# Kernel optimization log

Measured on AMD Instinct MI355X. Metric: run time of the kernel, lower is better.

Reference implementation:

```python
import jax, jax.numpy as jnp
import numpy as np

B, D, L, N = 16384, 128, 20, 1_000_000


def setup_inputs() -> dict:
    key = jax.random.key(0)
    k1, k2, k3, k4 = jax.random.split(key, 4)
    xw = jax.random.normal(k1, (B, D), dtype=jnp.float32)
    # weight table: row i == weight of nn.Linear(n_embs, 1) for node i
    W = jax.random.normal(k2, (N, D), dtype=jnp.float32) * 0.02
    h_path = jax.random.randint(k3, (L,), 0, N, dtype=jnp.int32)
    h_code = jax.random.randint(k4, (L,), 0, 2).astype(jnp.float32)
    return {"xw": xw, "W": W, "h_code": h_code, "h_path": h_path}


def reference(xw, W, h_code, h_path):
    # Gather only the L path rows (mirrors per-node tiny Linear lookups)
    Wp = W[h_path]                      # (L, D)
    z = jnp.einsum("bd,ld->bl", xw, Wp)  # (B, L) logits, one per path node
    # h_code*log(sigmoid(z)) + (1-h_code)*log(1-sigmoid(z)), computed stably:
    # log(sigmoid(z)) = log_sigmoid(z); log(1-sigmoid(z)) = log_sigmoid(-z)
    p = h_code * jax.nn.log_sigmoid(z) + (1.0 - h_code) * jax.nn.log_sigmoid(-z)
    # original sums the list of (B,1) tensors over the path
    return jnp.sum(p, axis=1, keepdims=True)  # (B, 1)
```

## Files before the change

### kernel.cpp

```cpp
#include <hip/hip_runtime.h>
#include <math.h>

#define BB 16384
#define DD 128
#define LL 20

__global__ __launch_bounds__(64) void hs_kernel(
    const float* __restrict__ xw,
    const float* __restrict__ W,
    const float* __restrict__ h_code,
    const int*   __restrict__ h_path,
    float* __restrict__ out)
{
    __shared__ float4 Ws[LL * (DD / 4)];
    __shared__ float  codes[LL];

    const int tid = threadIdx.x;

    for (int i = tid; i < LL * (DD / 4); i += 64) {
        const int l = i >> 5;
        const int c = i & 31;
        const long long row = (long long)h_path[l];
        Ws[i] = ((const float4*)W)[row * (DD / 4) + c];
    }
    if (tid < LL) codes[tid] = h_code[tid];
    __syncthreads();

    const int b = blockIdx.x * 64 + tid;
    const float4* x4 = (const float4*)(xw + (size_t)b * DD);

    float z[LL];
#pragma unroll
    for (int l = 0; l < LL; ++l) z[l] = 0.0f;

#pragma unroll 4
    for (int c = 0; c < DD / 4; ++c) {
        const float4 x = x4[c];
#pragma unroll
        for (int l = 0; l < LL; ++l) {
            const float4 w = Ws[l * (DD / 4) + c];
            z[l] += x.x * w.x + x.y * w.y + x.z * w.z + x.w * w.w;
        }
    }

    float s = 0.0f;
#pragma unroll
    for (int l = 0; l < LL; ++l) {
        const float zl = z[l];
        const float t  = -zl;
        const float sp = fmaxf(t, 0.0f) + log1pf(expf(-fabsf(t)));
        s -= sp + (1.0f - codes[l]) * zl;
    }
    out[b] = s;
}

extern "C" void kernel_launch(void* const* d_in, const int* in_sizes, int n_in,
                              void* d_out, int out_size, void* d_ws, size_t ws_size,
                              hipStream_t stream) {
    const float* xw     = (const float*)d_in[0];
    const float* W      = (const float*)d_in[1];
    const float* h_code = (const float*)d_in[2];
    const int*   h_path = (const int*)d_in[3];
    float* out = (float*)d_out;

    hs_kernel<<<BB / 64, 64, 0, stream>>>(xw, W, h_code, h_path, out);
}
```

Baseline: 567.3 us.

## Split each row's dot products across four threads with shuffle reduction

```diff
diff --git a/kernel.cpp b/kernel.cpp
--- a/kernel.cpp
+++ b/kernel.cpp
@@ -4,8 +4,10 @@
 #define BB 16384
 #define DD 128
 #define LL 20
+#define ROWS_PER_BLOCK 64
+#define THREADS 256
 
-__global__ __launch_bounds__(64) void hs_kernel(
+__global__ __launch_bounds__(THREADS) void hs_kernel(
     const float* __restrict__ xw,
     const float* __restrict__ W,
     const float* __restrict__ h_code,
@@ -17,24 +19,26 @@
 
     const int tid = threadIdx.x;
 
-    for (int i = tid; i < LL * (DD / 4); i += 64) {
+    for (int i = tid; i < LL * (DD / 4); i += THREADS) {
         const int l = i >> 5;
         const int c = i & 31;
-        const long long row = (long long)h_path[l];
-        Ws[i] = ((const float4*)W)[row * (DD / 4) + c];
+        Ws[i] = ((const float4*)W)[(long long)h_path[l] * (DD / 4) + c];
     }
     if (tid < LL) codes[tid] = h_code[tid];
     __syncthreads();
 
-    const int b = blockIdx.x * 64 + tid;
-    const float4* x4 = (const float4*)(xw + (size_t)b * DD);
+    const int p   = tid & 3;
+    const int r   = tid >> 2;
+    const int row = blockIdx.x * ROWS_PER_BLOCK + r;
+    const float4* x4 = (const float4*)xw + (size_t)row * (DD / 4);
 
     float z[LL];
 #pragma unroll
     for (int l = 0; l < LL; ++l) z[l] = 0.0f;
 
-#pragma unroll 4
-    for (int c = 0; c < DD / 4; ++c) {
+#pragma unroll
+    for (int j = 0; j < 8; ++j) {
+        const int c = p + 4 * j;
         const float4 x = x4[c];
 #pragma unroll
         for (int l = 0; l < LL; ++l) {
@@ -43,15 +47,23 @@
         }
     }
 
-    float s = 0.0f;
 #pragma unroll
     for (int l = 0; l < LL; ++l) {
-        const float zl = z[l];
-        const float t  = -zl;
-        const float sp = fmaxf(t, 0.0f) + log1pf(expf(-fabsf(t)));
-        s -= sp + (1.0f - codes[l]) * zl;
+        z[l] += __shfl_xor(z[l], 1);
+        z[l] += __shfl_xor(z[l], 2);
     }
-    out[b] = s;
+
+    if (p == 0) {
+        float s = 0.0f;
+#pragma unroll
+        for (int l = 0; l < LL; ++l) {
+            const float zl = z[l];
+            const float t  = -zl;
+            const float sp = fmaxf(t, 0.0f) + log1pf(expf(-fabsf(t)));
+            s -= sp + (1.0f - codes[l]) * zl;
+        }
+        out[row] = s;
+    }
 }
 
 extern "C" void kernel_launch(void* const* d_in, const int* in_sizes, int n_in,
@@ -63,5 +75,5 @@
     const int*   h_path = (const int*)d_in[3];
     float* out = (float*)d_out;
 
-    hs_kernel<<<BB / 64, 64, 0, stream>>>(xw, W, h_code, h_path, out);
+    hs_kernel<<<BB / ROWS_PER_BLOCK, THREADS, 0, stream>>>(xw, W, h_code, h_path, out);
 }
```

Measured after the change: 553.4 us. 1.03x faster.
